# Kernel optimization log

Hardware: AMD Instinct MI355X
Metric: run time of the kernel (lower is better)

The kernel has to match this reference:

```python
import jax, jax.numpy as jnp
import numpy as np

D_KEY, BANK_N = 128, 9720
BS, N = 1, 1620          # n = h*w = 30*54 (480p features, stride 16)
D_VAL, C, OBJ_N = 512, 512, 3


def setup_inputs() -> dict:
    key = jax.random.key(0)
    k1, k2, k3, k4, k5 = jax.random.split(key, 5)
    return {
        "keys_bank": jax.random.normal(k1, (D_KEY, BANK_N), dtype=jnp.float32),
        "q_in": jax.random.normal(k2, (BS, D_KEY, N), dtype=jnp.float32),
        "q_out": jax.random.normal(k3, (OBJ_N, C, N), dtype=jnp.float32),
        "values": jax.random.normal(k4, (OBJ_N, D_VAL, BANK_N), dtype=jnp.float32),
        "masks": jax.random.uniform(k5, (OBJ_N, 1, BANK_N), dtype=jnp.float32),
    }


def reference(keys_bank, q_in, q_out, values, masks):
    # p[b,k,n] = softmax_k( keys^T q_in / sqrt(d_key) )
    d_key = keys_bank.shape[0]
    scale = 1.0 / np.sqrt(d_key).astype(np.float32)
    p = jnp.einsum("dk,bdn->bkn", keys_bank, q_in) * scale
    p = jax.nn.softmax(p, axis=1)  # over bank dim

    # Batched over objects (original loops per object, sharing p)
    mem = jnp.einsum("ovk,bkn->obvn", values, p)       # (obj, bs, d_val, n)
    mask_mem = jnp.einsum("ouk,bkn->obun", masks, p)   # (obj, bs, 1, n)
    q_out_with_mask = q_out[:, None, :, :] * mask_mem  # (obj, bs, C, n)

    out = jnp.concatenate([mem, q_out_with_mask], axis=2)  # (obj, bs, d_val+C, n)
    return jnp.swapaxes(out, 0, 1)                          # (bs, obj, d_val+C, n)
```

## Files before the change

### kernel.cpp

```cpp
#include <hip/hip_runtime.h>
#include <hip/hip_bf16.h>

typedef unsigned short u16;
typedef unsigned char  u8;

#define D_KEY   128
#define BANK_N  9720
#define BANK_P  9728
#define N_TOK   1620
#define N_PAD   1664
#define OBJ_N   3
#define M_PAD   1664
#define LDCOL   1664
#define ONES_ROW 1539
#define QK_SCALE 0.08838834764831845f
#define KITERS  76

typedef __bf16 bf16x8 __attribute__((ext_vector_type(8)));
typedef float  f32x4  __attribute__((ext_vector_type(4)));
typedef unsigned int u32x4 __attribute__((ext_vector_type(4)));
typedef int i32x8 __attribute__((ext_vector_type(8)));

__device__ __forceinline__ float bf2f(u16 u) {
  union { unsigned int i; float f; } v; v.i = ((unsigned int)u) << 16; return v.f;
}
__device__ __forceinline__ u16 f2bf(float f) {
  unsigned int x = __float_as_uint(f);
  unsigned int r = x + 0x7fffu + ((x >> 16) & 1u);
  return (u16)(r >> 16);
}
__device__ __forceinline__ unsigned pack_fp8x4(float a, float b, float c, float d) {
  unsigned v = __builtin_amdgcn_cvt_pk_fp8_f32(a, b, 0, false);
  v = __builtin_amdgcn_cvt_pk_fp8_f32(c, d, v, true);
  return v;
}
__device__ __forceinline__ u8 f2fp8(float a) {
  return (u8)(__builtin_amdgcn_cvt_pk_fp8_f32(a, 0.f, 0, false) & 0xff);
}

__device__ __forceinline__ void load_lds16(const void* g, void* l) {
  __builtin_amdgcn_global_load_lds(
      (const __attribute__((address_space(1))) void*)g,
      (__attribute__((address_space(3))) void*)l, 16, 0, 0);
}

__global__ void prep(const float* __restrict__ q, const float* __restrict__ keys,
                     const float* __restrict__ values, const float* __restrict__ masks,
                     u16* __restrict__ qT, u16* __restrict__ kT, u8* __restrict__ vm8) {
  __shared__ float t[64][65];
  int b = blockIdx.x;
  if (b < 832) {
    int idx = b * 256 + threadIdx.x;
    int n = idx >> 7, d = idx & 127;
    float v = (n < N_TOK) ? q[d * N_TOK + n] * QK_SCALE : 0.f;
    qT[idx] = f2bf(v);
    return;
  }
  if (b < 1136) {
    b -= 832;
    const int bk = (b % 152) * 64;
    const int bd = (b / 152) * 64;
    const int tx = threadIdx.x & 63;
    const int ty = threadIdx.x >> 6;
#pragma unroll
    for (int i = 0; i < 64; i += 4) {
      int d = bd + ty + i;
      int k = bk + tx;
      t[ty + i][tx] = (k < BANK_N) ? keys[(size_t)d * BANK_N + k] : 0.f;
    }
    __syncthreads();
#pragma unroll
    for (int i = 0; i < 64; i += 4) {
      int r = ty + i;
      kT[(size_t)(bk + r) * D_KEY + bd + tx] = f2bf(t[tx][r]);
    }
    return;
  }
  const int NV = BANK_P / 4;
  int idx = (b - 1136) * 256 + threadIdx.x;
  if (idx >= M_PAD * NV) return;
  int m = idx / NV;
  int k4 = (idx - m * NV) * 4;
  float4 v = make_float4(0.f, 0.f, 0.f, 0.f);
  if (m == ONES_ROW) {
    v.x = (k4     < BANK_N) ? 1.f : 0.f;
    v.y = (k4 + 1 < BANK_N) ? 1.f : 0.f;
    v.z = (k4 + 2 < BANK_N) ? 1.f : 0.f;
    v.w = (k4 + 3 < BANK_N) ? 1.f : 0.f;
  } else {
    const float* src = nullptr;
    if (m < 1536)          src = values + (size_t)m * BANK_N;
    else if (m < ONES_ROW) src = masks + (size_t)(m - 1536) * BANK_N;
    if (src) {
      if (k4 + 3 < BANK_N) v = *(const float4*)(src + k4);
      else {
        if (k4     < BANK_N) v.x = src[k4];
        if (k4 + 1 < BANK_N) v.y = src[k4 + 1];
        if (k4 + 2 < BANK_N) v.z = src[k4 + 2];
        if (k4 + 3 < BANK_N) v.w = src[k4 + 3];
      }
    }
  }
  *(unsigned*)(vm8 + (size_t)m * BANK_P + k4) = pack_fp8x4(v.x, v.y, v.z, v.w);
}

__global__ void gemm_qk(const u16* __restrict__ A, const u16* __restrict__ B,
                        u8* __restrict__ E8)
{
  __shared__ __align__(16) u16 sbuf[8192];
  u16* As = sbuf;
  u16* Bs = sbuf + 4096;

  const int tid  = threadIdx.x;
  const int wave = tid >> 6;
  const int lane = tid & 63;
  const int bn = blockIdx.x % 76, bm = blockIdx.x / 76;

  const u16* Abase = A + (size_t)bm * 128 * D_KEY;
  const u16* Bbase = B + (size_t)bn * 128 * D_KEY;

  const int r  = lane >> 2;
  const int c8 = (lane & 3) << 3;
  const int s0 = wave, s1 = wave + 4;

  f32x4 acc[4][4];
#pragma unroll
  for (int i = 0; i < 4; i++)
#pragma unroll
    for (int j = 0; j < 4; j++) acc[i][j] = (f32x4){0.f, 0.f, 0.f, 0.f};

  const int m_in = lane & 15;
  const int quad = lane >> 4;
  const int wm = (wave >> 1) * 64;
  const int wn = (wave & 1) * 64;

  for (int kt = 0; kt < D_KEY; kt += 32) {
    load_lds16(Abase + (size_t)(s0 * 16 + r) * D_KEY + kt + c8, &As[s0 * 512]);
    load_lds16(Abase + (size_t)(s1 * 16 + r) * D_KEY + kt + c8, &As[s1 * 512]);
    load_lds16(Bbase + (size_t)(s0 * 16 + r) * D_KEY + kt + c8, &Bs[s0 * 512]);
    load_lds16(Bbase + (size_t)(s1 * 16 + r) * D_KEY + kt + c8, &Bs[s1 * 512]);
    __syncthreads();

    bf16x8 af[4], bfr[4];
#pragma unroll
    for (int i = 0; i < 4; i++)
      af[i] = *(const bf16x8*)&As[(wm + i * 16 + m_in) * 32 + quad * 8];
#pragma unroll
    for (int j = 0; j < 4; j++)
      bfr[j] = *(const bf16x8*)&Bs[(wn + j * 16 + m_in) * 32 + quad * 8];
#pragma unroll
    for (int i = 0; i < 4; i++)
#pragma unroll
      for (int j = 0; j < 4; j++)
        acc[i][j] = __builtin_amdgcn_mfma_f32_16x16x32_bf16(af[i], bfr[j], acc[i][j], 0, 0, 0);
    __syncthreads();
  }

  u8* sb8 = (u8*)sbuf;
#pragma unroll
  for (int i = 0; i < 4; i++)
#pragma unroll
    for (int j = 0; j < 4; j++)
#pragma unroll
      for (int t = 0; t < 4; t++) {
        int row_l = wm + i * 16 + quad * 4 + t;
        int col_l = wn + j * 16 + m_in;
        bool valid = (bn * 128 + col_l) < BANK_N;
        sb8[(row_l << 7) + col_l] = valid ? f2fp8(__expf(acc[i][j][t])) : (u8)0;
      }
  __syncthreads();

  for (int chunk = tid; chunk < 1024; chunk += 256) {
    int row = chunk >> 3;
    int cu  = (chunk & 7) << 4;
    u32x4 v = *(const u32x4*)&sb8[(row << 7) + cu];
    *(u32x4*)&E8[(size_t)(bm * 128 + row) * BANK_P + bn * 128 + cu] = v;
  }
}

__global__ __launch_bounds__(256, 3)
void gemm_pv(const u8* __restrict__ A, const u8* __restrict__ B,
             u16* __restrict__ memC, int nParts, size_t cPartStride)
{
  __shared__ __align__(16) u16 sbuf[16384];
  u8* As8 = (u8*)sbuf;
  u8* Bs8 = (u8*)sbuf + 16384;

  const int tid  = threadIdx.x;
  const int wave = tid >> 6;
  const int lane = tid & 63;

  const int bq = (int)gridDim.x >> 3, br = (int)gridDim.x & 7;
  const int xcd = blockIdx.x & 7, bj = blockIdx.x >> 3;
  int b = (xcd < br ? xcd * (bq + 1) : br * (bq + 1) + (xcd - br) * bq) + bj;

  int bz = b / 169;
  int rr = b - bz * 169;
  int gid = rr / 52;
  int rem = rr - gid * 52;
  int width = (gid < 3) ? 4 : 1;
  int bm = rem / width;
  int bn = gid * 4 + (rem - bm * width);

  const int base = KITERS / nParts;
  const int remP = KITERS - base * nParts;
  const int nt    = base + (bz < remP ? 1 : 0);
  const int itbeg = bz * base + (bz < remP ? bz : remP);
  const int kbeg  = itbeg * 128;

  const u8* Abase = A + (size_t)bm * 128 * BANK_P;
  const u8* Bbase = B + (size_t)bn * 128 * BANK_P;

  const int srow  = lane >> 1;
  const int shalf = (((lane & 1) ^ ((lane >> 3) & 1)) << 4);

  f32x4 acc[4][4];
#pragma unroll
  for (int i = 0; i < 4; i++)
#pragma unroll
    for (int j = 0; j < 4; j++) acc[i][j] = (f32x4){0.f, 0.f, 0.f, 0.f};

  const int m_in = lane & 15;
  const int quad = lane >> 4;
  const int wm = (wave >> 1) * 64;
  const int wn = (wave & 1) * 64;
  const int fxor = ((m_in >> 2) & 1) << 4;

  const size_t arow_off = (size_t)(wave * 32 + srow) * BANK_P;

  for (int it = 0; it < nt; ++it) {
    const int kt = kbeg + it * 128;
#pragma unroll
    for (int s = 0; s < 4; s++)
      load_lds16(Abase + arow_off + kt + s * 32 + shalf, As8 + s * 4096 + wave * 1024);
#pragma unroll
    for (int s = 0; s < 4; s++)
      load_lds16(Bbase + arow_off + kt + s * 32 + shalf, Bs8 + s * 4096 + wave * 1024);
    __syncthreads();

    i32x8 a8[4];
#pragma unroll
    for (int i = 0; i < 4; i++) {
      const u8* p = As8 + quad * 4096 + (wm + i * 16 + m_in) * 32;
      u32x4 lo = *(const u32x4*)(p + fxor);
      u32x4 hi = *(const u32x4*)(p + (fxor ^ 16));
      a8[i] = (i32x8){(int)lo[0], (int)lo[1], (int)lo[2], (int)lo[3],
                      (int)hi[0], (int)hi[1], (int)hi[2], (int)hi[3]};
    }
#pragma unroll
    for (int j = 0; j < 4; j++) {
      const u8* p = Bs8 + quad * 4096 + (wn + j * 16 + m_in) * 32;
      u32x4 lo = *(const u32x4*)(p + fxor);
      u32x4 hi = *(const u32x4*)(p + (fxor ^ 16));
      i32x8 b8 = (i32x8){(int)lo[0], (int)lo[1], (int)lo[2], (int)lo[3],
                         (int)hi[0], (int)hi[1], (int)hi[2], (int)hi[3]};
#pragma unroll
      for (int i = 0; i < 4; i++)
        acc[i][j] = __builtin_amdgcn_mfma_scale_f32_16x16x128_f8f6f4(
            a8[i], b8, acc[i][j], 0, 0,
            0, 0x7f7f7f7f, 0, 0x7f7f7f7f);
    }
    __syncthreads();
  }

  u16* Cg = memC + (size_t)bz * cPartStride;
#pragma unroll
  for (int h = 0; h < 2; h++) {
    __syncthreads();
    if ((wave >> 1) == h) {
#pragma unroll
      for (int i = 0; i < 4; i++)
#pragma unroll
        for (int j = 0; j < 4; j++)
#pragma unroll
          for (int t = 0; t < 4; t++) {
            int row_l = i * 16 + quad * 4 + t;
            int col_l = wn + j * 16 + m_in;
            sbuf[(row_l << 7) + col_l] = f2bf(acc[i][j][t]);
          }
    }
    __syncthreads();
    for (int chunk = tid; chunk < 1024; chunk += 256) {
      int row = chunk >> 4;
      int cu  = (chunk & 15) << 3;
      u32x4 v = *(const u32x4*)&sbuf[(row << 7) + cu];
      __builtin_nontemporal_store(
          v, (u32x4*)&Cg[(size_t)(bm * 128 + h * 64 + row) * LDCOL + bn * 128 + cu]);
    }
  }
}

__global__ void epilogue(const u16* __restrict__ memC, const float* __restrict__ q_out,
                         float* __restrict__ out, int nParts) {
  const int NV = N_TOK / 4;
  int idx = blockIdx.x * 256 + threadIdx.x;
  if (idx >= OBJ_N * 1024 * NV) return;
  int n4 = (idx % NV) * 4;
  int t = idx / NV;
  int c = t & 1023;
  int o = t >> 10;
  const size_t ps = (size_t)M_PAD * LDCOL;

  const u16* lbase = memC + (size_t)ONES_ROW * LDCOL + n4;
  float4 l = make_float4(0.f, 0.f, 0.f, 0.f);
  for (int z = 0; z < nParts; z++) {
    ushort4 v = *(const ushort4*)(lbase + z * ps);
    l.x += bf2f(v.x); l.y += bf2f(v.y); l.z += bf2f(v.z); l.w += bf2f(v.w);
  }

  size_t rowoff = (c < 512) ? (size_t)(o * 512 + c) * LDCOL
                            : (size_t)(1536 + o) * LDCOL;
  const u16* base = memC + rowoff + n4;
  float4 s = make_float4(0.f, 0.f, 0.f, 0.f);
  for (int z = 0; z < nParts; z++) {
    ushort4 v = *(const ushort4*)(base + z * ps);
    s.x += bf2f(v.x); s.y += bf2f(v.y); s.z += bf2f(v.z); s.w += bf2f(v.w);
  }
  float4 rv;
  float ix = 1.f / l.x, iy = 1.f / l.y, iz = 1.f / l.z, iw = 1.f / l.w;
  if (c < 512) {
    rv.x = s.x * ix; rv.y = s.y * iy; rv.z = s.z * iz; rv.w = s.w * iw;
  } else {
    float4 q = *(const float4*)(q_out + (size_t)(o * 512 + (c - 512)) * N_TOK + n4);
    rv.x = q.x * s.x * ix; rv.y = q.y * s.y * iy;
    rv.z = q.z * s.z * iz; rv.w = q.w * s.w * iw;
  }
  *(float4*)(out + (size_t)(o * 1024 + c) * N_TOK + n4) = rv;
}

extern "C" void kernel_launch(void* const* d_in, const int* in_sizes, int n_in,
                              void* d_out, int out_size, void* d_ws, size_t ws_size,
                              hipStream_t stream) {
  const float* keys   = (const float*)d_in[0];
  const float* q_in   = (const float*)d_in[1];
  const float* q_out  = (const float*)d_in[2];
  const float* values = (const float*)d_in[3];
  const float* masks  = (const float*)d_in[4];
  float* out = (float*)d_out;

  char* ws = (char*)d_ws;
  size_t off = 0;
  auto alloc = [&](size_t bytes) -> void* {
    void* p = ws + off; off += (bytes + 255) & ~(size_t)255; return p;
  };
  u16* qT  = (u16*)alloc((size_t)N_PAD * D_KEY * 2);
  u16* kT  = (u16*)alloc((size_t)BANK_P * D_KEY * 2);
  u8*  vm8 = (u8*)alloc((size_t)M_PAD * BANK_P);
  u8*  E8  = (u8*)alloc((size_t)N_PAD * BANK_P);

  int nParts = 8;
  while (nParts > 1 && off + (size_t)nParts * M_PAD * LDCOL * 2 > ws_size) nParts >>= 1;
  u16* memC = (u16*)alloc((size_t)nParts * M_PAD * LDCOL * 2);

  const int vmBlocks = (M_PAD * (BANK_P / 4) + 255) / 256;
  prep<<<1136 + vmBlocks, 256, 0, stream>>>(q_in, keys, values, masks, qT, kT, vm8);

  gemm_qk<<<988, 256, 0, stream>>>(qT, kT, E8);

  gemm_pv<<<dim3(169 * nParts), 256, 0, stream>>>(vm8, E8, memC, nParts, (size_t)M_PAD * LDCOL);

  epilogue<<<(OBJ_N * 1024 * (N_TOK / 4) + 255) / 256, 256, 0, stream>>>(
      memC, q_out, out, nParts);
}
```

Baseline: 195.2 us.

## Tile q transpose, widen fp8 packing, precompute softmax denominators once

The q transpose in prep now uses LDS tiles, so global reads are coalesced instead of strided. The values/masks fp8 packing has each thread handle 16 elements and issue one 16-byte store. A new small kernel reduces the softmax denominator row across partitions once and stores reciprocals, so the epilogue no longer repeats that reduction and division for every output row. The cost is one extra kernel launch and a small workspace buffer.

New measurement: 198.0 us. About the same (+1.4%).

```diff
diff --git a/kernel.cpp b/kernel.cpp
--- a/kernel.cpp
+++ b/kernel.cpp
@@ -49,19 +49,29 @@
                      u16* __restrict__ qT, u16* __restrict__ kT, u8* __restrict__ vm8) {
   __shared__ float t[64][65];
   int b = blockIdx.x;
-  if (b < 832) {
-    int idx = b * 256 + threadIdx.x;
-    int n = idx >> 7, d = idx & 127;
-    float v = (n < N_TOK) ? q[d * N_TOK + n] * QK_SCALE : 0.f;
-    qT[idx] = f2bf(v);
+  const int tx = threadIdx.x & 63;
+  const int ty = threadIdx.x >> 6;
+  if (b < 52) {
+    const int bd = (b & 1) * 64;
+    const int bn = (b >> 1) * 64;
+#pragma unroll
+    for (int i = 0; i < 64; i += 4) {
+      int d = bd + ty + i;
+      int n = bn + tx;
+      t[ty + i][tx] = (n < N_TOK) ? q[(size_t)d * N_TOK + n] : 0.f;
+    }
+    __syncthreads();
+#pragma unroll
+    for (int i = 0; i < 64; i += 4) {
+      int r = ty + i;
+      qT[(size_t)(bn + r) * D_KEY + bd + tx] = f2bf(t[tx][r] * QK_SCALE);
+    }
     return;
   }
-  if (b < 1136) {
-    b -= 832;
+  if (b < 356) {
+    b -= 52;
     const int bk = (b % 152) * 64;
     const int bd = (b / 152) * 64;
-    const int tx = threadIdx.x & 63;
-    const int ty = threadIdx.x >> 6;
 #pragma unroll
     for (int i = 0; i < 64; i += 4) {
       int d = bd + ty + i;
@@ -76,22 +86,26 @@
     }
     return;
   }
-  const int NV = BANK_P / 4;
-  int idx = (b - 1136) * 256 + threadIdx.x;
+  const int NV = BANK_P / 16;
+  int idx = (b - 356) * 256 + threadIdx.x;
   if (idx >= M_PAD * NV) return;
   int m = idx / NV;
-  int k4 = (idx - m * NV) * 4;
-  float4 v = make_float4(0.f, 0.f, 0.f, 0.f);
-  if (m == ONES_ROW) {
-    v.x = (k4     < BANK_N) ? 1.f : 0.f;
-    v.y = (k4 + 1 < BANK_N) ? 1.f : 0.f;
-    v.z = (k4 + 2 < BANK_N) ? 1.f : 0.f;
-    v.w = (k4 + 3 < BANK_N) ? 1.f : 0.f;
-  } else {
-    const float* src = nullptr;
-    if (m < 1536)          src = values + (size_t)m * BANK_N;
-    else if (m < ONES_ROW) src = masks + (size_t)(m - 1536) * BANK_N;
-    if (src) {
+  int k16 = (idx - m * NV) * 16;
+  const bool ones = (m == ONES_ROW);
+  const float* src = nullptr;
+  if (m < 1536)          src = values + (size_t)m * BANK_N;
+  else if (m < ONES_ROW) src = masks + (size_t)(m - 1536) * BANK_N;
+  u32x4 outv;
+#pragma unroll
+  for (int c = 0; c < 4; c++) {
+    int k4 = k16 + c * 4;
+    float4 v = make_float4(0.f, 0.f, 0.f, 0.f);
+    if (ones) {
+      v.x = (k4     < BANK_N) ? 1.f : 0.f;
+      v.y = (k4 + 1 < BANK_N) ? 1.f : 0.f;
+      v.z = (k4 + 2 < BANK_N) ? 1.f : 0.f;
+      v.w = (k4 + 3 < BANK_N) ? 1.f : 0.f;
+    } else if (src) {
       if (k4 + 3 < BANK_N) v = *(const float4*)(src + k4);
       else {
         if (k4     < BANK_N) v.x = src[k4];
@@ -100,8 +114,9 @@
         if (k4 + 3 < BANK_N) v.w = src[k4 + 3];
       }
     }
-  }
-  *(unsigned*)(vm8 + (size_t)m * BANK_P + k4) = pack_fp8x4(v.x, v.y, v.z, v.w);
+    outv[c] = pack_fp8x4(v.x, v.y, v.z, v.w);
+  }
+  *(u32x4*)(vm8 + (size_t)m * BANK_P + k16) = outv;
 }
 
 __global__ void gemm_qk(const u16* __restrict__ A, const u16* __restrict__ B,
@@ -290,8 +305,20 @@
   }
 }
 
+__global__ void lsum_inv_k(const u16* __restrict__ memC, float* __restrict__ inv_l,
+                           int nParts) {
+  int n = blockIdx.x * 256 + threadIdx.x;
+  if (n >= N_TOK) return;
+  const size_t ps = (size_t)M_PAD * LDCOL;
+  const u16* p = memC + (size_t)ONES_ROW * LDCOL + n;
+  float s = 0.f;
+  for (int z = 0; z < nParts; z++) s += bf2f(p[(size_t)z * ps]);
+  inv_l[n] = 1.f / s;
+}
+
 __global__ void epilogue(const u16* __restrict__ memC, const float* __restrict__ q_out,
-                         float* __restrict__ out, int nParts) {
+                         const float* __restrict__ inv_l, float* __restrict__ out,
+                         int nParts) {
   const int NV = N_TOK / 4;
   int idx = blockIdx.x * 256 + threadIdx.x;
   if (idx >= OBJ_N * 1024 * NV) return;
@@ -301,12 +328,7 @@
   int o = t >> 10;
   const size_t ps = (size_t)M_PAD * LDCOL;
 
-  const u16* lbase = memC + (size_t)ONES_ROW * LDCOL + n4;
-  float4 l = make_float4(0.f, 0.f, 0.f, 0.f);
-  for (int z = 0; z < nParts; z++) {
-    ushort4 v = *(const ushort4*)(lbase + z * ps);
-    l.x += bf2f(v.x); l.y += bf2f(v.y); l.z += bf2f(v.z); l.w += bf2f(v.w);
-  }
+  float4 il = *(const float4*)(inv_l + n4);
 
   size_t rowoff = (c < 512) ? (size_t)(o * 512 + c) * LDCOL
                             : (size_t)(1536 + o) * LDCOL;
@@ -317,13 +339,12 @@
     s.x += bf2f(v.x); s.y += bf2f(v.y); s.z += bf2f(v.z); s.w += bf2f(v.w);
   }
   float4 rv;
-  float ix = 1.f / l.x, iy = 1.f / l.y, iz = 1.f / l.z, iw = 1.f / l.w;
   if (c < 512) {
-    rv.x = s.x * ix; rv.y = s.y * iy; rv.z = s.z * iz; rv.w = s.w * iw;
+    rv.x = s.x * il.x; rv.y = s.y * il.y; rv.z = s.z * il.z; rv.w = s.w * il.w;
   } else {
     float4 q = *(const float4*)(q_out + (size_t)(o * 512 + (c - 512)) * N_TOK + n4);
-    rv.x = q.x * s.x * ix; rv.y = q.y * s.y * iy;
-    rv.z = q.z * s.z * iz; rv.w = q.w * s.w * iw;
+    rv.x = q.x * s.x * il.x; rv.y = q.y * s.y * il.y;
+    rv.z = q.z * s.z * il.z; rv.w = q.w * s.w * il.w;
   }
   *(float4*)(out + (size_t)(o * 1024 + c) * N_TOK + n4) = rv;
 }
@@ -343,22 +364,25 @@
   auto alloc = [&](size_t bytes) -> void* {
     void* p = ws + off; off += (bytes + 255) & ~(size_t)255; return p;
   };
-  u16* qT  = (u16*)alloc((size_t)N_PAD * D_KEY * 2);
-  u16* kT  = (u16*)alloc((size_t)BANK_P * D_KEY * 2);
-  u8*  vm8 = (u8*)alloc((size_t)M_PAD * BANK_P);
-  u8*  E8  = (u8*)alloc((size_t)N_PAD * BANK_P);
+  u16*  qT    = (u16*)alloc((size_t)N_PAD * D_KEY * 2);
+  u16*  kT    = (u16*)alloc((size_t)BANK_P * D_KEY * 2);
+  u8*   vm8   = (u8*)alloc((size_t)M_PAD * BANK_P);
+  u8*   E8    = (u8*)alloc((size_t)N_PAD * BANK_P);
+  float* inv_l = (float*)alloc((size_t)N_PAD * 4);
 
   int nParts = 8;
   while (nParts > 1 && off + (size_t)nParts * M_PAD * LDCOL * 2 > ws_size) nParts >>= 1;
   u16* memC = (u16*)alloc((size_t)nParts * M_PAD * LDCOL * 2);
 
-  const int vmBlocks = (M_PAD * (BANK_P / 4) + 255) / 256;
-  prep<<<1136 + vmBlocks, 256, 0, stream>>>(q_in, keys, values, masks, qT, kT, vm8);
+  const int vmBlocks = (M_PAD * (BANK_P / 16) + 255) / 256;
+  prep<<<356 + vmBlocks, 256, 0, stream>>>(q_in, keys, values, masks, qT, kT, vm8);
 
   gemm_qk<<<988, 256, 0, stream>>>(qT, kT, E8);
 
   gemm_pv<<<dim3(169 * nParts), 256, 0, stream>>>(vm8, E8, memC, nParts, (size_t)M_PAD * LDCOL);
 
+  lsum_inv_k<<<(N_TOK + 255) / 256, 256, 0, stream>>>(memC, inv_l, nParts);
+
   epilogue<<<(OBJ_N * 1024 * (N_TOK / 4) + 255) / 256, 256, 0, stream>>>(
-      memC, q_out, out, nParts);
-}
+      memC, q_out, inv_l, out, nParts);
+}
```
